# Kernel optimization log

Measured on AMD Instinct MI355X. Metric: run time of the kernel, lower is better.

Reference implementation:

```python
import jax, jax.numpy as jnp
import numpy as np

B = 4096
N_ENTITY = 100000
N_USER = 10000
N_RELATION = 32
DIM = 64
N_ITER = 2
K = 16  # n_neighbors


def setup_inputs() -> dict:
    key = jax.random.key(0)
    ks = jax.random.split(key, 8)
    pairs = jax.random.randint(ks[0], (B, 2), 0, N_USER, dtype=jnp.int64 if jax.config.jax_enable_x64 else jnp.int32)
    adj_entity = jax.random.randint(ks[1], (N_ENTITY, K), 0, N_ENTITY)
    adj_relation = jax.random.randint(ks[2], (N_ENTITY, K), 0, N_RELATION)
    # xavier_uniform-style scale for embeddings
    def xavier(k, shape):
        limit = float(np.sqrt(6.0 / (shape[0] + shape[1])))
        return jax.random.uniform(k, shape, jnp.float32, -limit, limit)
    entity_emb = xavier(ks[3], (N_ENTITY, DIM))
    relation_emb = xavier(ks[4], (N_RELATION, DIM))
    user_emb = xavier(ks[5], (N_USER, DIM))
    W = xavier(ks[6], (DIM, DIM))
    b = jnp.zeros((DIM,), jnp.float32)
    return {"pairs": pairs, "adj_entity": adj_entity, "adj_relation": adj_relation,
            "entity_emb": entity_emb, "relation_emb": relation_emb,
            "user_emb": user_emb, "W": W, "b": b}


def reference(pairs, adj_entity, adj_relation, entity_emb, relation_emb, user_emb, W, b):
    n = pairs.shape[0]
    dim = entity_emb.shape[1]
    k = adj_entity.shape[1]
    users = pairs[:, 0]
    items = pairs[:, 1]

    # multi-hop neighbor expansion (mirrors get_neighbors)
    entities = [items]
    relations = []
    for i in range(N_ITER):
        entities.append(adj_entity[entities[i]].reshape(-1))
        relations.append(adj_relation[entities[i]].reshape(-1))

    u = user_emb[users]  # [B, D]
    ev = [entity_emb[entities[i]].reshape(n, -1, dim) for i in range(N_ITER + 1)]
    rv = [relation_emb[relations[i]].reshape(n, -1, dim) for i in range(N_ITER)]

    for l in range(N_ITER):
        nxt = []
        for i in range(N_ITER - l):
            r = rv[i].reshape(n, -1, k, dim)          # [B, M, K, D]
            scores = jnp.einsum('bd,bmkd->bmk', u, r) # user-relation attention
            attn = jax.nn.softmax(scores, axis=-1)[..., None]
            nbr = (attn * ev[i + 1].reshape(n, -1, k, dim)).sum(axis=-2)  # [B, M, D]
            x = ev[i].reshape(n, -1, dim) + nbr       # residual add
            h = x @ W.T + b                            # Linear(dim, dim)
            nxt.append(jnp.tanh(h) if l == N_ITER - 1 else jax.nn.relu(h))
        ev = nxt

    item_embeddings = ev[0].reshape(-1, dim)  # [B, D]
    return jax.nn.sigmoid(jnp.sum(u * item_embeddings, axis=1))
```

## Files before the change

### kernel.cpp

```cpp
#include <hip/hip_runtime.h>
#include <hip/hip_bf16.h>
#include <math.h>

#define DIM  64
#define KN   16
#define NREL 32

__device__ __forceinline__ float frcp(float x) { return __builtin_amdgcn_rcpf(x); }

__device__ __forceinline__ unsigned short f2bf(float f) {
    unsigned u = __float_as_uint(f);
    u = (u + 0x7fffu + ((u >> 16) & 1u)) >> 16;
    return (unsigned short)u;
}
__device__ __forceinline__ float bf2f(unsigned short b) {
    return __uint_as_float((unsigned)b << 16);
}

__global__ __launch_bounds__(256, 4) void we_kernel(
    const float* __restrict__ entity_emb,
    const float* __restrict__ W,
    unsigned short* __restrict__ WEb,
    int nRows)
{
    __shared__ float4 xs_s[4][8 * 16];
    const int tid  = threadIdx.x;
    const int wave = tid >> 6;
    const int lane = tid & 63;
    float4* xs = xs_s[wave];

    const int base = (blockIdx.x * 4 + wave) * 8;
    if (base >= nRows) return;

    float4 Wr[16];
    const float4* W4 = (const float4*)(W + lane * DIM);
    #pragma unroll
    for (int j = 0; j < 16; ++j) Wr[j] = W4[j];

    const float4* src = (const float4*)entity_emb;
    #pragma unroll
    for (int i = 0; i < 2; ++i) {
        const int idx = i * 64 + lane;
        const int row = base + (idx >> 4);
        const size_t g = (row < nRows) ? ((size_t)base * 16 + idx) : 0;
        xs[idx] = src[g];
    }
    asm volatile("s_waitcnt lgkmcnt(0)" ::: "memory");

    #pragma unroll
    for (int r = 0; r < 8; ++r) {
        const int row = base + r;
        if (row >= nRows) break;
        float h0 = 0.f, h1 = 0.f, h2 = 0.f, h3 = 0.f;
        #pragma unroll
        for (int jc = 0; jc < 16; jc += 4) {
            float4 a = xs[r * 16 + jc + 0];
            float4 b = xs[r * 16 + jc + 1];
            float4 c = xs[r * 16 + jc + 2];
            float4 d = xs[r * 16 + jc + 3];
            h0 += a.x*Wr[jc+0].x + a.y*Wr[jc+0].y + a.z*Wr[jc+0].z + a.w*Wr[jc+0].w;
            h1 += b.x*Wr[jc+1].x + b.y*Wr[jc+1].y + b.z*Wr[jc+1].z + b.w*Wr[jc+1].w;
            h2 += c.x*Wr[jc+2].x + c.y*Wr[jc+2].y + c.z*Wr[jc+2].z + c.w*Wr[jc+2].w;
            h3 += d.x*Wr[jc+3].x + d.y*Wr[jc+3].y + d.z*Wr[jc+3].z + d.w*Wr[jc+3].w;
        }
        WEb[(size_t)row * DIM + lane] = f2bf((h0 + h1) + (h2 + h3));
    }
}

__global__ __launch_bounds__(256, 4) void kgcn_main(
    const int* __restrict__ pairs,
    const int* __restrict__ adjE,
    const int* __restrict__ adjR,
    const unsigned short* __restrict__ WEb,
    const float* __restrict__ relation_emb,
    const float* __restrict__ user_emb,
    const float* __restrict__ W,
    const float* __restrict__ bias,
    float* __restrict__ out,
    int nPairs)
{
    __shared__ float ev1_s[4][KN * DIM];
    __shared__ float xb_s[4][DIM];

    const int tid  = threadIdx.x;
    const int wave = tid >> 6;
    const int lane = tid & 63;
    const int p    = blockIdx.x * 4 + wave;
    if (p >= nPairs) return;

    float* ev1 = ev1_s[wave];
    float* xb  = xb_s[wave];

    const int user = pairs[2 * p + 0];
    const int item = pairs[2 * p + 1];

    const float bval = bias[lane];
    const float uval = user_emb[(size_t)user * DIM + lane];
    const unsigned short* WE_l = WEb + lane;

    int rk0 = 0, e1 = 0;
    if (lane < KN) {
        rk0 = adjR[(size_t)item * KN + lane];
        e1  = adjE[(size_t)item * KN + lane];
    }

    float acc;
    {
        const int r = lane >> 1, hlf = lane & 1;
        const float4* rel4 = (const float4*)(relation_emb + r * DIM + hlf * 32);
        const float4* u4   = (const float4*)(user_emb + (size_t)user * DIM + hlf * 32);
        float a0 = 0.f, a1 = 0.f;
        #pragma unroll
        for (int j = 0; j < 8; j += 2) {
            float4 a = rel4[j],     b = u4[j];
            float4 c = rel4[j + 1], d = u4[j + 1];
            a0 += a.x*b.x + a.y*b.y + a.z*b.z + a.w*b.w;
            a1 += c.x*d.x + c.y*d.y + c.z*d.z + c.w*d.w;
        }
        acc = a0 + a1;
        acc += __shfl_xor(acc, 1);
    }

    auto softmax16 = [&](float s) -> float {
        float mx = s;
        mx = fmaxf(mx, __shfl_xor(mx, 1));
        mx = fmaxf(mx, __shfl_xor(mx, 2));
        mx = fmaxf(mx, __shfl_xor(mx, 4));
        mx = fmaxf(mx, __shfl_xor(mx, 8));
        float e = __expf(s - mx);
        float ss = e;
        ss += __shfl_xor(ss, 1);
        ss += __shfl_xor(ss, 2);
        ss += __shfl_xor(ss, 4);
        ss += __shfl_xor(ss, 8);
        return e * frcp(ss);
    };

    const float w0 = softmax16(__shfl(acc, rk0 << 1));

    const int m4 = lane >> 4, kk = lane & 15;
    int ekA[4]; float wA[4];
    #pragma unroll
    for (int c = 0; c < 4; ++c) {
        const int g  = __shfl(e1, 4 * c + m4);
        const int rk = adjR[(size_t)(unsigned)g * KN + kk];
        ekA[c]       = adjE[(size_t)(unsigned)g * KN + kk];
        wA[c] = softmax16(__shfl(acc, rk << 1));
    }

    #pragma unroll 2
    for (int m = 0; m < KN; ++m) {
        const int c   = m >> 2;
        const int sub = (m & 3) * 16;
        const int g   = __shfl(e1, m);
        float ha = bf2f(WE_l[(size_t)(unsigned)g * DIM]) + bval;
        float hb = 0.f;
        #pragma unroll
        for (int k = 0; k < KN; k += 2) {
            const int   ea = __shfl(ekA[c], sub + k);
            const float fa = __shfl(wA[c],  sub + k);
            const int   eb = __shfl(ekA[c], sub + k + 1);
            const float fb = __shfl(wA[c],  sub + k + 1);
            ha += fa * bf2f(WE_l[(size_t)(unsigned)ea * DIM]);
            hb += fb * bf2f(WE_l[(size_t)(unsigned)eb * DIM]);
        }
        ev1[m * DIM + lane] = fmaxf(ha + hb, 0.f);
    }

    float ha = bf2f(WE_l[(size_t)item * DIM]) + bval;
    float hb = 0.f;
    #pragma unroll
    for (int k = 0; k < KN; k += 2) {
        const int   ea = __shfl(e1, k);
        const float fa = __shfl(w0, k);
        const int   eb = __shfl(e1, k + 1);
        const float fb = __shfl(w0, k + 1);
        ha += fa * bf2f(WE_l[(size_t)(unsigned)ea * DIM]);
        hb += fb * bf2f(WE_l[(size_t)(unsigned)eb * DIM]);
    }
    const float e0 = fmaxf(ha + hb, 0.f);

    asm volatile("s_waitcnt lgkmcnt(0)" ::: "memory");
    float xa = e0, xc = 0.f;
    #pragma unroll
    for (int k = 0; k < KN; k += 2) {
        xa += __shfl(w0, k)     * ev1[k * DIM + lane];
        xc += __shfl(w0, k + 1) * ev1[(k + 1) * DIM + lane];
    }
    const float x1 = xa + xc;

    asm volatile("s_waitcnt lgkmcnt(0)" ::: "memory");
    xb[lane] = x1;
    asm volatile("s_waitcnt lgkmcnt(0)" ::: "memory");
    float h0 = bval, h1 = 0.f, h2 = 0.f, h3 = 0.f;
    {
        const float4* Wl  = (const float4*)(W + lane * DIM);
        const float4* xv4 = (const float4*)xb;
        #pragma unroll
        for (int j = 0; j < 16; j += 4) {
            float4 w0v = Wl[j],   x0v = xv4[j];
            float4 w1v = Wl[j+1], x1v = xv4[j+1];
            float4 w2v = Wl[j+2], x2v = xv4[j+2];
            float4 w3v = Wl[j+3], x3v = xv4[j+3];
            h0 += w0v.x*x0v.x + w0v.y*x0v.y + w0v.z*x0v.z + w0v.w*x0v.w;
            h1 += w1v.x*x1v.x + w1v.y*x1v.y + w1v.z*x1v.z + w1v.w*x1v.w;
            h2 += w2v.x*x2v.x + w2v.y*x2v.y + w2v.z*x2v.z + w2v.w*x2v.w;
            h3 += w3v.x*x3v.x + w3v.y*x3v.y + w3v.z*x3v.z + w3v.w*x3v.w;
        }
    }
    const float itemf = tanhf((h0 + h1) + (h2 + h3));

    float d = uval * itemf;
    d += __shfl_xor(d, 1);
    d += __shfl_xor(d, 2);
    d += __shfl_xor(d, 4);
    d += __shfl_xor(d, 8);
    d += __shfl_xor(d, 16);
    d += __shfl_xor(d, 32);
    if (lane == 0) out[p] = 1.f / (1.f + expf(-d));
}

__global__ __launch_bounds__(256, 4) void kgcn_fallback(
    const int* __restrict__ pairs, const int* __restrict__ adj_entity,
    const int* __restrict__ adj_relation, const float* __restrict__ entity_emb,
    const float* __restrict__ relation_emb, const float* __restrict__ user_emb,
    const float* __restrict__ W, const float* __restrict__ bias,
    float* __restrict__ out, int nPairs)
{
    __shared__ float ev1_s[2][KN * DIM];
    __shared__ float xb_s[4][DIM];
    const int tid = threadIdx.x, wave = tid >> 6, lane = tid & 63;
    const int q = wave >> 1, half = wave & 1;
    int p = blockIdx.x * 2 + q;
    if (p >= nPairs) p = nPairs - 1;
    float* ev1 = ev1_s[q]; float* xb = xb_s[wave];
    const int user = pairs[2 * p + 0], item = pairs[2 * p + 1];
    const float bval = bias[lane];
    const float* emb_l = entity_emb + lane;
    const float4* W4 = (const float4*)(W + lane * DIM);
    int rk0 = 0, e1 = 0;
    if (lane < KN) {
        rk0 = adj_relation[(size_t)item * KN + lane];
        e1  = adj_entity[(size_t)item * KN + lane];
    }
    float acc;
    {
        const int r = lane >> 1, hlf = lane & 1;
        const float4* rel4 = (const float4*)(relation_emb + r * DIM + hlf * 32);
        const float4* u4 = (const float4*)(user_emb + (size_t)user * DIM + hlf * 32);
        float a0 = 0.f, a1 = 0.f;
        #pragma unroll
        for (int j = 0; j < 8; j += 2) {
            float4 a = rel4[j], b = u4[j], c = rel4[j+1], d = u4[j+1];
            a0 += a.x*b.x + a.y*b.y + a.z*b.z + a.w*b.w;
            a1 += c.x*d.x + c.y*d.y + c.z*d.z + c.w*d.w;
        }
        acc = a0 + a1; acc += __shfl_xor(acc, 1);
    }
    auto softmax16 = [&](float s) -> float {
        float mx = s;
        mx = fmaxf(mx, __shfl_xor(mx, 1)); mx = fmaxf(mx, __shfl_xor(mx, 2));
        mx = fmaxf(mx, __shfl_xor(mx, 4)); mx = fmaxf(mx, __shfl_xor(mx, 8));
        float e = __expf(s - mx);
        float ss = e;
        ss += __shfl_xor(ss, 1); ss += __shfl_xor(ss, 2);
        ss += __shfl_xor(ss, 4); ss += __shfl_xor(ss, 8);
        return e * frcp(ss);
    };
    auto matvec = [&](float xv) -> float {
        asm volatile("s_waitcnt lgkmcnt(0)" ::: "memory");
        xb[lane] = xv;
        asm volatile("s_waitcnt lgkmcnt(0)" ::: "memory");
        float h0 = bval, h1 = 0.f, h2 = 0.f, h3 = 0.f;
        const float4* xv4 = (const float4*)xb;
        #pragma unroll
        for (int j = 0; j < 16; j += 4) {
            float4 w0 = W4[j], x0 = xv4[j], w1 = W4[j+1], x1 = xv4[j+1];
            float4 w2 = W4[j+2], x2 = xv4[j+2], w3 = W4[j+3], x3 = xv4[j+3];
            h0 += w0.x*x0.x + w0.y*x0.y + w0.z*x0.z + w0.w*x0.w;
            h1 += w1.x*x1.x + w1.y*x1.y + w1.z*x1.z + w1.w*x1.w;
            h2 += w2.x*x2.x + w2.y*x2.y + w2.z*x2.z + w2.w*x2.w;
            h3 += w3.x*x3.x + w3.y*x3.y + w3.z*x3.z + w3.w*x3.w;
        }
        return (h0 + h1) + (h2 + h3);
    };
    auto gather = [&](int self, int ek, float w) -> float {
        float xa = emb_l[(size_t)(unsigned)self * DIM], xc = 0.f;
        #pragma unroll
        for (int k = 0; k < KN; k += 2) {
            const int e0i = __shfl(ek, k); const float f0 = __shfl(w, k);
            const int e1i = __shfl(ek, k + 1); const float f1 = __shfl(w, k + 1);
            xa += f0 * emb_l[(size_t)(unsigned)e0i * DIM];
            xc += f1 * emb_l[(size_t)(unsigned)e1i * DIM];
        }
        return xa + xc;
    };
    int rk_n = 0, ek_n = 0;
    {
        const int g0 = __shfl(e1, half * 8);
        if (lane < KN) {
            rk_n = adj_relation[(size_t)(unsigned)g0 * KN + lane];
            ek_n = adj_entity[(size_t)(unsigned)g0 * KN + lane];
        }
    }
    #pragma unroll 1
    for (int mi = 0; mi < 8; ++mi) {
        const int m = half * 8 + mi;
        const int g = __shfl(e1, m);
        const int rk = rk_n, ek = ek_n;
        if (mi + 1 < 8) {
            const int gn = __shfl(e1, m + 1);
            if (lane < KN) {
                rk_n = adj_relation[(size_t)(unsigned)gn * KN + lane];
                ek_n = adj_entity[(size_t)(unsigned)gn * KN + lane];
            }
        }
        const float w = softmax16(__shfl(acc, rk << 1));
        const float x = gather(g, ek, w);
        ev1[m * DIM + lane] = fmaxf(matvec(x), 0.f);
    }
    __syncthreads();
    if (half != 0) return;
    const float w0 = softmax16(__shfl(acc, rk0 << 1));
    const float x0 = gather(item, e1, w0);
    const float e0 = fmaxf(matvec(x0), 0.f);
    float xa = e0, xc = 0.f;
    #pragma unroll
    for (int k = 0; k < KN; k += 2) {
        xa += __shfl(w0, k) * ev1[k * DIM + lane];
        xc += __shfl(w0, k + 1) * ev1[(k + 1) * DIM + lane];
    }
    const float itemf = tanhf(matvec(xa + xc));
    float d = user_emb[(size_t)user * DIM + lane] * itemf;
    d += __shfl_xor(d, 1); d += __shfl_xor(d, 2); d += __shfl_xor(d, 4);
    d += __shfl_xor(d, 8); d += __shfl_xor(d, 16); d += __shfl_xor(d, 32);
    if (lane == 0) out[p] = 1.f / (1.f + expf(-d));
}

extern "C" void kernel_launch(void* const* d_in, const int* in_sizes, int n_in,
                              void* d_out, int out_size, void* d_ws, size_t ws_size,
                              hipStream_t stream) {
    const int*   pairs        = (const int*)d_in[0];
    const int*   adj_entity   = (const int*)d_in[1];
    const int*   adj_relation = (const int*)d_in[2];
    const float* entity_emb   = (const float*)d_in[3];
    const float* relation_emb = (const float*)d_in[4];
    const float* user_emb     = (const float*)d_in[5];
    const float* W            = (const float*)d_in[6];
    const float* b            = (const float*)d_in[7];
    float* out = (float*)d_out;

    const int nPairs = in_sizes[0] / 2;
    const int nEnt   = in_sizes[3] / DIM;
    const size_t weBytes = (size_t)in_sizes[3] * sizeof(unsigned short);

    if (ws_size >= weBytes) {
        unsigned short* WEb = (unsigned short*)d_ws;
        const int preBlocks = (nEnt + 8 * 4 - 1) / (8 * 4);
        we_kernel<<<preBlocks, 256, 0, stream>>>(entity_emb, W, WEb, nEnt);
        const int mainBlocks = (nPairs + 3) / 4;
        kgcn_main<<<mainBlocks, 256, 0, stream>>>(pairs, adj_entity, adj_relation,
                                                  WEb, relation_emb, user_emb,
                                                  W, b, out, nPairs);
    } else {
        const int nBlocks = (nPairs + 1) / 2;
        kgcn_fallback<<<nBlocks, 256, 0, stream>>>(pairs, adj_entity, adj_relation,
                                                   entity_emb, relation_emb, user_emb,
                                                   W, b, out, nPairs);
    }
}
```

Before: 154.8 us.

## Gather bf16 pairs per lane and split wave halves across neighbor rows

Each lane now loads two packed bf16 values with a single 32-bit load, and the two half-waves handle different neighbor rows (or different halves of the K loop), combining results with a cross-half shuffle. This halves the number of gather load instructions and doubles the bytes fetched per load, aiming to cut memory-instruction and latency cost in the random-gather stage. In exchange it adds reduction shuffles, and the m loop is no longer unrolled, which may reduce memory-level parallelism.

New measurement: 147.6 us. 1.05x faster.

```diff
diff --git a/kernel.cpp b/kernel.cpp
--- a/kernel.cpp
+++ b/kernel.cpp
@@ -13,9 +13,8 @@
     u = (u + 0x7fffu + ((u >> 16) & 1u)) >> 16;
     return (unsigned short)u;
 }
-__device__ __forceinline__ float bf2f(unsigned short b) {
-    return __uint_as_float((unsigned)b << 16);
-}
+__device__ __forceinline__ float bflo(unsigned v) { return __uint_as_float(v << 16); }
+__device__ __forceinline__ float bfhi(unsigned v) { return __uint_as_float(v & 0xffff0000u); }
 
 __global__ __launch_bounds__(256, 4) void we_kernel(
     const float* __restrict__ entity_emb,
@@ -91,12 +90,15 @@
     float* ev1 = ev1_s[wave];
     float* xb  = xb_s[wave];
 
+    const int h  = lane >> 5;
+    const int c  = lane & 31;
+    const int c2 = c * 2;
+
     const int user = pairs[2 * p + 0];
     const int item = pairs[2 * p + 1];
 
-    const float bval = bias[lane];
-    const float uval = user_emb[(size_t)user * DIM + lane];
-    const unsigned short* WE_l = WEb + lane;
+    const float2 b2 = *(const float2*)(bias + c2);
+    const unsigned* WErow = (const unsigned*)WEb;
 
     int rk0 = 0, e1 = 0;
     if (lane < KN) {
@@ -113,9 +115,9 @@
         #pragma unroll
         for (int j = 0; j < 8; j += 2) {
             float4 a = rel4[j],     b = u4[j];
-            float4 c = rel4[j + 1], d = u4[j + 1];
+            float4 cc = rel4[j + 1], d = u4[j + 1];
             a0 += a.x*b.x + a.y*b.y + a.z*b.z + a.w*b.w;
-            a1 += c.x*d.x + c.y*d.y + c.z*d.z + c.w*d.w;
+            a1 += cc.x*d.x + cc.y*d.y + cc.z*d.z + cc.w*d.w;
         }
         acc = a0 + a1;
         acc += __shfl_xor(acc, 1);
@@ -141,58 +143,68 @@
     const int m4 = lane >> 4, kk = lane & 15;
     int ekA[4]; float wA[4];
     #pragma unroll
-    for (int c = 0; c < 4; ++c) {
-        const int g  = __shfl(e1, 4 * c + m4);
+    for (int s = 0; s < 4; ++s) {
+        const int g  = __shfl(e1, 4 * s + m4);
         const int rk = adjR[(size_t)(unsigned)g * KN + kk];
-        ekA[c]       = adjE[(size_t)(unsigned)g * KN + kk];
-        wA[c] = softmax16(__shfl(acc, rk << 1));
-    }
-
-    #pragma unroll 2
-    for (int m = 0; m < KN; ++m) {
-        const int c   = m >> 2;
-        const int sub = (m & 3) * 16;
-        const int g   = __shfl(e1, m);
-        float ha = bf2f(WE_l[(size_t)(unsigned)g * DIM]) + bval;
-        float hb = 0.f;
-        #pragma unroll
-        for (int k = 0; k < KN; k += 2) {
-            const int   ea = __shfl(ekA[c], sub + k);
-            const float fa = __shfl(wA[c],  sub + k);
-            const int   eb = __shfl(ekA[c], sub + k + 1);
-            const float fb = __shfl(wA[c],  sub + k + 1);
-            ha += fa * bf2f(WE_l[(size_t)(unsigned)ea * DIM]);
-            hb += fb * bf2f(WE_l[(size_t)(unsigned)eb * DIM]);
-        }
-        ev1[m * DIM + lane] = fmaxf(ha + hb, 0.f);
-    }
-
-    float ha = bf2f(WE_l[(size_t)item * DIM]) + bval;
-    float hb = 0.f;
-    #pragma unroll
-    for (int k = 0; k < KN; k += 2) {
-        const int   ea = __shfl(e1, k);
-        const float fa = __shfl(w0, k);
-        const int   eb = __shfl(e1, k + 1);
-        const float fb = __shfl(w0, k + 1);
-        ha += fa * bf2f(WE_l[(size_t)(unsigned)ea * DIM]);
-        hb += fb * bf2f(WE_l[(size_t)(unsigned)eb * DIM]);
-    }
-    const float e0 = fmaxf(ha + hb, 0.f);
+        ekA[s]       = adjE[(size_t)(unsigned)g * KN + kk];
+        wA[s] = softmax16(__shfl(acc, rk << 1));
+    }
+
+    #pragma unroll 1
+    for (int m = 0; m < KN; m += 2) {
+        const int s    = m >> 2;
+        const int subh = ((m & 3) + h) * 16;
+        const int gs   = __shfl(e1, m + h);
+        unsigned sv = WErow[(size_t)(unsigned)gs * 32 + c];
+        float ax = b2.x + bflo(sv);
+        float ay = b2.y + bfhi(sv);
+        #pragma unroll
+        for (int k = 0; k < KN; ++k) {
+            const int   e = __shfl(ekA[s], subh + k);
+            const float w = __shfl(wA[s],  subh + k);
+            unsigned v = WErow[(size_t)(unsigned)e * 32 + c];
+            ax += w * bflo(v);
+            ay += w * bfhi(v);
+        }
+        *(float2*)&ev1[(m + h) * DIM + c2] = make_float2(fmaxf(ax, 0.f), fmaxf(ay, 0.f));
+    }
+
+    float ax = 0.f, ay = 0.f;
+    #pragma unroll
+    for (int k = 0; k < 8; ++k) {
+        const int   e = __shfl(e1, h * 8 + k);
+        const float w = __shfl(w0, h * 8 + k);
+        unsigned v = WErow[(size_t)(unsigned)e * 32 + c];
+        ax += w * bflo(v);
+        ay += w * bfhi(v);
+    }
+    ax += __shfl_xor(ax, 32);
+    ay += __shfl_xor(ay, 32);
+    {
+        unsigned sv = WErow[(size_t)item * 32 + c];
+        ax += bflo(sv) + b2.x;
+        ay += bfhi(sv) + b2.y;
+    }
+    const float e0x = fmaxf(ax, 0.f), e0y = fmaxf(ay, 0.f);
 
     asm volatile("s_waitcnt lgkmcnt(0)" ::: "memory");
-    float xa = e0, xc = 0.f;
-    #pragma unroll
-    for (int k = 0; k < KN; k += 2) {
-        xa += __shfl(w0, k)     * ev1[k * DIM + lane];
-        xc += __shfl(w0, k + 1) * ev1[(k + 1) * DIM + lane];
-    }
-    const float x1 = xa + xc;
+    float sx = 0.f, sy = 0.f;
+    #pragma unroll
+    for (int k = 0; k < 8; ++k) {
+        const int   kg = h * 8 + k;
+        const float w  = __shfl(w0, kg);
+        float2 ev = *(const float2*)&ev1[kg * DIM + c2];
+        sx += w * ev.x;
+        sy += w * ev.y;
+    }
+    sx += __shfl_xor(sx, 32);
+    sy += __shfl_xor(sy, 32);
+    const float x1x = e0x + sx, x1y = e0y + sy;
 
     asm volatile("s_waitcnt lgkmcnt(0)" ::: "memory");
-    xb[lane] = x1;
+    if (h == 0) *(float2*)&xb[c2] = make_float2(x1x, x1y);
     asm volatile("s_waitcnt lgkmcnt(0)" ::: "memory");
-    float h0 = bval, h1 = 0.f, h2 = 0.f, h3 = 0.f;
+    float h0 = bias[lane], h1 = 0.f, h2 = 0.f, h3 = 0.f;
     {
         const float4* Wl  = (const float4*)(W + lane * DIM);
         const float4* xv4 = (const float4*)xb;
@@ -210,7 +222,7 @@
     }
     const float itemf = tanhf((h0 + h1) + (h2 + h3));
 
-    float d = uval * itemf;
+    float d = user_emb[(size_t)user * DIM + lane] * itemf;
     d += __shfl_xor(d, 1);
     d += __shfl_xor(d, 2);
     d += __shfl_xor(d, 4);
```
